# Optimization experiments

Measured on AMD Instinct MI355X. Metric: run time of the kernel, lower is better.

## Reference

```python
import jax, jax.numpy as jnp
import numpy as np

N, F_IN, F_OUT = 2048, 128, 64


def setup_inputs() -> dict:
    key = jax.random.key(0)
    k0, k1, k2, k3, k4 = jax.random.split(key, 5)
    node_features = jax.random.normal(k0, (N, F_IN), dtype=jnp.float32)
    adjacency_matrix = jax.random.uniform(k1, (N, N), dtype=jnp.float32)
    mask_father = jax.random.uniform(k2, (N, N), dtype=jnp.float32)
    mask_hadamard = jax.random.uniform(k3, (N, N), dtype=jnp.float32)
    # kaiming_uniform (fan_in, relu): bound = sqrt(6 / fan_in) * sqrt(2) adjustment -> gain*sqrt(3/fan_in)
    bound = np.sqrt(2.0) * np.sqrt(3.0 / F_IN)
    weight = jax.random.uniform(k4, (F_IN, F_OUT), dtype=jnp.float32, minval=-bound, maxval=bound)
    bias = jnp.zeros((F_OUT,), dtype=jnp.float32)
    return {
        "node_features": node_features,
        "adjacency_matrix": adjacency_matrix,
        "mask_father": mask_father,
        "mask_hadamard": mask_hadamard,
        "weight": weight,
        "bias": bias,
    }


def reference(node_features, adjacency_matrix, mask_father, mask_hadamard, weight, bias):
    # H[i,f] = (X @ W + b)[i,f]
    H = node_features @ weight + bias  # [N, F]
    # Original math: out[j,f] = sum_k mf[j,k] * H[k,f] * (sum_i A[j,i] * H[i,f] * mh[i,k])
    # G[j,f,k] corresponds to the (masked hadamard @ adjacency) intermediate [N, F, N]
    G = jnp.einsum('ji,if,ik->jfk', adjacency_matrix, H, mask_hadamard)
    out = jnp.einsum('jfk,kf,jk->jf', G, H, mask_father)
    return out
```

## Files before the change

kernel.cpp:

```cpp
#include <hip/hip_runtime.h>
#include <hip/hip_bf16.h>


typedef __attribute__((ext_vector_type(8))) _Float16 f16x8;
typedef __attribute__((ext_vector_type(4))) _Float16 f16x4;
typedef __attribute__((ext_vector_type(4))) float f32x4;

#define N 2048
#define FOUT 64
#define FIN 128
#define BI 64
#define NIT 512

__device__ __forceinline__ void gl_lds16(const _Float16* g, _Float16* l) {
    __builtin_amdgcn_global_load_lds(
        (const __attribute__((address_space(1))) void*)g,
        (__attribute__((address_space(3))) void*)l, 16, 0, 0);
}


__global__ __launch_bounds__(256) void k_h(const float* __restrict__ X,
                                           const float* __restrict__ W,
                                           const float* __restrict__ bias,
                                           float* __restrict__ HT,
                                           _Float16* __restrict__ HTh) {
    __shared__ float Ws[FIN * FOUT];
    __shared__ float Xs[4 * FIN];
    int t = threadIdx.x;
#pragma unroll
    for (int s = 0; s < 32; ++s) Ws[t + 256 * s] = W[t + 256 * s];
    int i0 = blockIdx.x * 4;
#pragma unroll
    for (int s = 0; s < 2; ++s) { int idx = t + 256 * s; Xs[idx] = X[(size_t)i0 * FIN + idx]; }
    __syncthreads();
    int f = t & 63, il = t >> 6;
    float h = bias[f];
#pragma unroll
    for (int p = 0; p < FIN; ++p) h = fmaf(Xs[il * FIN + p], Ws[p * FOUT + f], h);
    int i = i0 + il;
    HT[f * N + i] = h;
    HTh[f * N + i] = (_Float16)h;
}

__global__ __launch_bounds__(256) void k_a2h(const float* __restrict__ A,
                                             _Float16* __restrict__ Ah) {
    int g = blockIdx.x * 256 + threadIdx.x;
    float4 v = ((const float4*)A)[g];
    f16x4 o;
    o[0] = (_Float16)v.x; o[1] = (_Float16)v.y; o[2] = (_Float16)v.z; o[3] = (_Float16)v.w;
    ((f16x4*)Ah)[g] = o;
}

__global__ __launch_bounds__(256) void k_mht(const float* __restrict__ mh,
                                             _Float16* __restrict__ mhT) {
    __shared__ float tile[64][65];
    int t = threadIdx.x;
    int bx = blockIdx.x & 31;
    int by = blockIdx.x >> 5;
#pragma unroll
    for (int s = 0; s < 16; ++s) {
        int lin = t + 256 * s;
        int r = lin >> 6, c = lin & 63;
        tile[r][c] = mh[(size_t)(by * 64 + r) * N + bx * 64 + c];
    }
    __syncthreads();
#pragma unroll
    for (int s = 0; s < 16; ++s) {
        int lin = t + 256 * s;
        int kr = lin >> 6, ic = lin & 63;
        mhT[(size_t)(bx * 64 + kr) * N + by * 64 + ic] = (_Float16)tile[ic][kr];
    }
}

__global__ __launch_bounds__(256, 2) void k_main(const float* __restrict__ mf,
                                                 const float* __restrict__ HT,
                                                 const _Float16* __restrict__ HTh,
                                                 const _Float16* __restrict__ Ah,
                                                 const _Float16* __restrict__ mhT,
                                                 float* __restrict__ out) {
    __shared__ _Float16 tiles[2][2][128 * BI];
    __shared__ _Float16 hbuf[2][N];
    __shared__ float red[2][4][64];

    int t = threadIdx.x;
    int jbase = (blockIdx.x >> 5) << 7;
    int f0 = (blockIdx.x & 31) << 1;
    int w = t >> 6, lane = t & 63, q = lane >> 4, l16 = lane & 15;
    int wj = (w & 1) << 6, wk = (w >> 1) << 6;

#pragma unroll
    for (int s = 0; s < 2; ++s) {
        int idx = t + 256 * s;
        ((f16x8*)hbuf)[idx] = *(const f16x8*)&HTh[(size_t)(f0 + (idx >> 8)) * N + (idx & 255) * 8];
    }

    int lrow = lane >> 3;
    int lchunk = (lane & 7) ^ lrow;
    int a_base = (jbase + w * 32 + lrow) * N + lchunk * 8;
    int b_base = (w * 32 + lrow) * N + lchunk * 8;
    int lds_w = w * 2048;

    float outp[2][4][4];
#pragma unroll
    for (int fi = 0; fi < 2; ++fi)
#pragma unroll
        for (int a = 0; a < 4; ++a)
#pragma unroll
            for (int b = 0; b < 4; ++b) outp[fi][a][b] = 0.f;

    {
        const _Float16* pa = Ah + a_base;
        const _Float16* pb = mhT + b_base;
        _Float16* la = &tiles[0][0][lds_w];
        _Float16* lb = &tiles[0][1][lds_w];
#pragma unroll
        for (int c = 0; c < 4; ++c) {
            gl_lds16(pa + c * 8 * N, la + c * 512);
            gl_lds16(pb + c * 8 * N, lb + c * 512);
        }
    }

    f32x4 acc[2][4][4];
#pragma unroll
    for (int fi = 0; fi < 2; ++fi)
#pragma unroll
        for (int a = 0; a < 4; ++a)
#pragma unroll
            for (int b = 0; b < 4; ++b) acc[fi][a][b] = (f32x4){0.f, 0.f, 0.f, 0.f};

    for (int it = 0; it < NIT; ++it) {
        int buf = it & 1;
        int ibase = (it & 31) << 6;
        int kbase = (it >> 5) << 7;

        __syncthreads();

        if (it + 1 < NIT) {
            int ib2 = ((it + 1) & 31) << 6;
            int kt2 = (it + 1) >> 5;
            const _Float16* pa = Ah + a_base + ib2;
            const _Float16* pb = mhT + b_base + kt2 * 128 * N + ib2;
            _Float16* la = &tiles[buf ^ 1][0][lds_w];
            _Float16* lb = &tiles[buf ^ 1][1][lds_w];
#pragma unroll
            for (int c = 0; c < 4; ++c) {
                gl_lds16(pa + c * 8 * N, la + c * 512);
                gl_lds16(pb + c * 8 * N, lb + c * 512);
            }
        }

        const _Float16* ta = tiles[buf][0];
        const _Float16* tb = tiles[buf][1];
#pragma unroll
        for (int s = 0; s < 2; ++s) {
            f16x8 ar[4], br[4];
#pragma unroll
            for (int x = 0; x < 4; ++x) {
                int row = wj + x * 16 + l16;
                ar[x] = *(const f16x8*)&ta[row * 64 + (((q + 4 * s) ^ (l16 & 7)) * 8)];
            }
#pragma unroll
            for (int x = 0; x < 4; ++x) {
                int row = wk + x * 16 + l16;
                br[x] = *(const f16x8*)&tb[row * 64 + (((q + 4 * s) ^ (l16 & 7)) * 8)];
            }
            f16x8 h0 = *(const f16x8*)&hbuf[0][ibase + s * 32 + q * 8];
            f16x8 h1 = *(const f16x8*)&hbuf[1][ibase + s * 32 + q * 8];
#pragma unroll
            for (int jj = 0; jj < 4; ++jj) {
                f16x8 a0 = ar[jj] * h0;
                f16x8 a1 = ar[jj] * h1;
#pragma unroll
                for (int kk = 0; kk < 4; ++kk) {
                    acc[0][jj][kk] = __builtin_amdgcn_mfma_f32_16x16x32_f16(a0, br[kk], acc[0][jj][kk], 0, 0, 0);
                    acc[1][jj][kk] = __builtin_amdgcn_mfma_f32_16x16x32_f16(a1, br[kk], acc[1][jj][kk], 0, 0, 0);
                }
            }
        }

        if ((it & 31) == 31) {
#pragma unroll
            for (int jj = 0; jj < 4; ++jj) {
                float t0[4] = {0.f, 0.f, 0.f, 0.f};
                float t1[4] = {0.f, 0.f, 0.f, 0.f};
#pragma unroll
                for (int kk = 0; kk < 4; ++kk) {
                    int kg = kbase + wk + kk * 16 + l16;
                    float hk0 = HT[f0 * N + kg];
                    float hk1 = HT[(f0 + 1) * N + kg];
                    int jrow = jbase + wj + jj * 16 + q * 4;
#pragma unroll
                    for (int r = 0; r < 4; ++r) {
                        float m = mf[(size_t)(jrow + r) * N + kg];
                        t0[r] = fmaf(acc[0][jj][kk][r], m * hk0, t0[r]);
                        t1[r] = fmaf(acc[1][jj][kk][r], m * hk1, t1[r]);
                    }
                }
#pragma unroll
                for (int r = 0; r < 4; ++r) {
                    float v0 = t0[r], v1 = t1[r];
                    v0 += __shfl_xor(v0, 1); v1 += __shfl_xor(v1, 1);
                    v0 += __shfl_xor(v0, 2); v1 += __shfl_xor(v1, 2);
                    v0 += __shfl_xor(v0, 4); v1 += __shfl_xor(v1, 4);
                    v0 += __shfl_xor(v0, 8); v1 += __shfl_xor(v1, 8);
                    outp[0][jj][r] += v0;
                    outp[1][jj][r] += v1;
                }
            }
#pragma unroll
            for (int fi = 0; fi < 2; ++fi)
#pragma unroll
                for (int a = 0; a < 4; ++a)
#pragma unroll
                    for (int b = 0; b < 4; ++b) acc[fi][a][b] = (f32x4){0.f, 0.f, 0.f, 0.f};
        }
    }

    if (l16 == 0) {
#pragma unroll
        for (int fi = 0; fi < 2; ++fi)
#pragma unroll
            for (int jj = 0; jj < 4; ++jj)
#pragma unroll
                for (int r = 0; r < 4; ++r)
                    red[fi][w][jj * 16 + q * 4 + r] = outp[fi][jj][r];
    }
    __syncthreads();
    if (t < 128) {
        int j = t;
#pragma unroll
        for (int fi = 0; fi < 2; ++fi) {
            float v = (j < 64) ? (red[fi][0][j] + red[fi][2][j])
                               : (red[fi][1][j - 64] + red[fi][3][j - 64]);
            out[(size_t)(jbase + j) * FOUT + f0 + fi] = v;
        }
    }
}

extern "C" void kernel_launch(void* const* d_in, const int* in_sizes, int n_in,
                              void* d_out, int out_size, void* d_ws, size_t ws_size,
                              hipStream_t stream) {
    const float* X    = (const float*)d_in[0];
    const float* A    = (const float*)d_in[1];
    const float* mf   = (const float*)d_in[2];
    const float* mh   = (const float*)d_in[3];
    const float* W    = (const float*)d_in[4];
    const float* bias = (const float*)d_in[5];
    float* out = (float*)d_out;

    float*    HT  = (float*)d_ws;
    _Float16* HTh = (_Float16*)((char*)d_ws + 524288);
    _Float16* Ah  = (_Float16*)((char*)d_ws + 1048576);
    _Float16* mhT = (_Float16*)((char*)d_ws + 1048576 + 8388608);

    k_h<<<N / 4, 256, 0, stream>>>(X, W, bias, HT, HTh);
    k_a2h<<<(N * N / 4) / 256, 256, 0, stream>>>(A, Ah);
    k_mht<<<(N / 64) * (N / 64), 256, 0, stream>>>(mh, mhT);
    k_main<<<16 * 32, 256, 0, stream>>>(mf, HT, HTh, Ah, mhT, out);
}
```

Baseline: 1.015 ms.

## Interleave async LDS prefetch with MFMA phases using explicit barriers and priority

```diff
diff --git a/kernel.cpp b/kernel.cpp
--- a/kernel.cpp
+++ b/kernel.cpp
@@ -11,6 +11,11 @@
 #define FIN 128
 #define BI 64
 #define NIT 512
+
+#define MFMA16(A,B,C) __builtin_amdgcn_mfma_f32_16x16x32_f16((A),(B),(C),0,0,0)
+#define BARS  { __builtin_amdgcn_s_barrier(); __builtin_amdgcn_sched_barrier(0); }
+#define LGKM0 { asm volatile("s_waitcnt lgkmcnt(0)" ::: "memory"); __builtin_amdgcn_sched_barrier(0); }
+#define VM0   { asm volatile("s_waitcnt vmcnt(0)" ::: "memory"); __builtin_amdgcn_sched_barrier(0); }
 
 __device__ __forceinline__ void gl_lds16(const _Float16* g, _Float16* l) {
     __builtin_amdgcn_global_load_lds(
@@ -128,55 +133,100 @@
 #pragma unroll
             for (int b = 0; b < 4; ++b) acc[fi][a][b] = (f32x4){0.f, 0.f, 0.f, 0.f};
 
+    __syncthreads();
+
     for (int it = 0; it < NIT; ++it) {
         int buf = it & 1;
         int ibase = (it & 31) << 6;
         int kbase = (it >> 5) << 7;
-
-        __syncthreads();
-
-        if (it + 1 < NIT) {
-            int ib2 = ((it + 1) & 31) << 6;
-            int kt2 = (it + 1) >> 5;
-            const _Float16* pa = Ah + a_base + ib2;
-            const _Float16* pb = mhT + b_base + kt2 * 128 * N + ib2;
-            _Float16* la = &tiles[buf ^ 1][0][lds_w];
-            _Float16* lb = &tiles[buf ^ 1][1][lds_w];
-#pragma unroll
-            for (int c = 0; c < 4; ++c) {
-                gl_lds16(pa + c * 8 * N, la + c * 512);
-                gl_lds16(pb + c * 8 * N, lb + c * 512);
-            }
-        }
-
         const _Float16* ta = tiles[buf][0];
         const _Float16* tb = tiles[buf][1];
-#pragma unroll
-        for (int s = 0; s < 2; ++s) {
-            f16x8 ar[4], br[4];
-#pragma unroll
-            for (int x = 0; x < 4; ++x) {
-                int row = wj + x * 16 + l16;
-                ar[x] = *(const f16x8*)&ta[row * 64 + (((q + 4 * s) ^ (l16 & 7)) * 8)];
-            }
-#pragma unroll
-            for (int x = 0; x < 4; ++x) {
-                int row = wk + x * 16 + l16;
-                br[x] = *(const f16x8*)&tb[row * 64 + (((q + 4 * s) ^ (l16 & 7)) * 8)];
-            }
-            f16x8 h0 = *(const f16x8*)&hbuf[0][ibase + s * 32 + q * 8];
-            f16x8 h1 = *(const f16x8*)&hbuf[1][ibase + s * 32 + q * 8];
-#pragma unroll
-            for (int jj = 0; jj < 4; ++jj) {
-                f16x8 a0 = ar[jj] * h0;
-                f16x8 a1 = ar[jj] * h1;
-#pragma unroll
-                for (int kk = 0; kk < 4; ++kk) {
-                    acc[0][jj][kk] = __builtin_amdgcn_mfma_f32_16x16x32_f16(a0, br[kk], acc[0][jj][kk], 0, 0, 0);
-                    acc[1][jj][kk] = __builtin_amdgcn_mfma_f32_16x16x32_f16(a1, br[kk], acc[1][jj][kk], 0, 0, 0);
-                }
-            }
-        }
+        bool more = (it + 1 < NIT);
+        int ib2 = ((it + 1) & 31) << 6;
+        int kt2 = (it + 1) >> 5;
+        const _Float16* pa = Ah + a_base + ib2;
+        const _Float16* pb = mhT + b_base + kt2 * 128 * N + ib2;
+        _Float16* la = &tiles[buf ^ 1][0][lds_w];
+        _Float16* lb = &tiles[buf ^ 1][1][lds_w];
+
+        VM0
+        BARS
+
+        f16x8 ar0[4], br0[4];
+#pragma unroll
+        for (int x = 0; x < 4; ++x)
+            ar0[x] = *(const f16x8*)&ta[(wj + x * 16 + l16) * 64 + ((q ^ (l16 & 7)) * 8)];
+#pragma unroll
+        for (int x = 0; x < 4; ++x)
+            br0[x] = *(const f16x8*)&tb[(wk + x * 16 + l16) * 64 + ((q ^ (l16 & 7)) * 8)];
+        f16x8 h00 = *(const f16x8*)&hbuf[0][ibase + q * 8];
+        f16x8 h10 = *(const f16x8*)&hbuf[1][ibase + q * 8];
+        if (more) {
+            gl_lds16(pa + 0 * 8 * N, la + 0 * 512);
+            gl_lds16(pb + 0 * 8 * N, lb + 0 * 512);
+            gl_lds16(pa + 1 * 8 * N, la + 1 * 512);
+            gl_lds16(pb + 1 * 8 * N, lb + 1 * 512);
+        }
+        BARS
+        LGKM0
+        __builtin_amdgcn_s_setprio(1);
+#pragma unroll
+        for (int jj = 0; jj < 4; ++jj) {
+            f16x8 a0 = ar0[jj] * h00;
+#pragma unroll
+            for (int kk = 0; kk < 4; ++kk)
+                acc[0][jj][kk] = MFMA16(a0, br0[kk], acc[0][jj][kk]);
+        }
+        __builtin_amdgcn_s_setprio(0);
+
+        if (more) {
+            gl_lds16(pa + 2 * 8 * N, la + 2 * 512);
+            gl_lds16(pb + 2 * 8 * N, lb + 2 * 512);
+            gl_lds16(pa + 3 * 8 * N, la + 3 * 512);
+            gl_lds16(pb + 3 * 8 * N, lb + 3 * 512);
+        }
+        BARS
+        __builtin_amdgcn_s_setprio(1);
+#pragma unroll
+        for (int jj = 0; jj < 4; ++jj) {
+            f16x8 a1 = ar0[jj] * h10;
+#pragma unroll
+            for (int kk = 0; kk < 4; ++kk)
+                acc[1][jj][kk] = MFMA16(a1, br0[kk], acc[1][jj][kk]);
+        }
+        __builtin_amdgcn_s_setprio(0);
+
+        f16x8 ar1[4], br1[4];
+#pragma unroll
+        for (int x = 0; x < 4; ++x)
+            ar1[x] = *(const f16x8*)&ta[(wj + x * 16 + l16) * 64 + (((q + 4) ^ (l16 & 7)) * 8)];
+#pragma unroll
+        for (int x = 0; x < 4; ++x)
+            br1[x] = *(const f16x8*)&tb[(wk + x * 16 + l16) * 64 + (((q + 4) ^ (l16 & 7)) * 8)];
+        f16x8 h01 = *(const f16x8*)&hbuf[0][ibase + 32 + q * 8];
+        f16x8 h11 = *(const f16x8*)&hbuf[1][ibase + 32 + q * 8];
+        BARS
+        LGKM0
+        __builtin_amdgcn_s_setprio(1);
+#pragma unroll
+        for (int jj = 0; jj < 4; ++jj) {
+            f16x8 a0 = ar1[jj] * h01;
+#pragma unroll
+            for (int kk = 0; kk < 4; ++kk)
+                acc[0][jj][kk] = MFMA16(a0, br1[kk], acc[0][jj][kk]);
+        }
+        __builtin_amdgcn_s_setprio(0);
+
+        BARS
+        __builtin_amdgcn_s_setprio(1);
+#pragma unroll
+        for (int jj = 0; jj < 4; ++jj) {
+            f16x8 a1 = ar1[jj] * h11;
+#pragma unroll
+            for (int kk = 0; kk < 4; ++kk)
+                acc[1][jj][kk] = MFMA16(a1, br1[kk], acc[1][jj][kk]);
+        }
+        __builtin_amdgcn_s_setprio(0);
 
         if ((it & 31) == 31) {
 #pragma unroll
```

After: 1.020 ms. About the same (+0.5%).
